# Kernel optimization log

Hardware: AMD Instinct MI355X
Metric: run time of the kernel (lower is better)

## Reference

```python
import jax, jax.numpy as jnp
import numpy as np

# Model dims
B, T, D = 1, 2048, 2048          # batch, seq_len, d_model
HI, DI = 4, 64                   # indexer heads / dim
H, DH = 16, 128                  # attention heads / head dim (H*DH == D)
TOPK = 512                       # sparse top-k tokens per query
NEG = -1e9


def setup_inputs() -> dict:
    key = jax.random.key(0)
    ks = jax.random.split(key, 8)
    s = 0.02  # weight init scale
    return {
        "hidden_states": jax.random.normal(ks[0], (B, T, D), jnp.float32),
        "Wq_idx": jax.random.normal(ks[1], (D, HI * DI), jnp.float32) * s,
        "Wk_idx": jax.random.normal(ks[2], (D, DI), jnp.float32) * s,
        "Ww_idx": jax.random.normal(ks[3], (D, HI), jnp.float32) * s,
        "Wq": jax.random.normal(ks[4], (D, H * DH), jnp.float32) * s,
        "Wk": jax.random.normal(ks[5], (D, H * DH), jnp.float32) * s,
        "Wv": jax.random.normal(ks[6], (D, H * DH), jnp.float32) * s,
        "Wo": jax.random.normal(ks[7], (H * DH, D), jnp.float32) * s,
    }


def reference(hidden_states, Wq_idx, Wk_idx, Ww_idx, Wq, Wk, Wv, Wo):
    x = hidden_states
    # ---- Lightning indexer: I[t,s] = sum_j w[t,j] * relu(q[t,j] . k[s]) ----
    qi = (x @ Wq_idx).reshape(B, T, HI, DI)          # [B,T,HI,DI]
    ki = x @ Wk_idx                                   # [B,S,DI]
    w = x @ Ww_idx                                    # [B,T,HI]
    dots = jnp.einsum('bthd,bsd->bths', qi, ki)       # [B,T,HI,S]
    index_scores = (jax.nn.relu(dots) * w[..., None]).sum(axis=2)  # [B,T,S]

    # ---- Top-k token selection with causal mask ----
    causal = jnp.triu(jnp.ones((T, T), dtype=bool), 1)            # True above diag
    masked_scores = jnp.where(causal[None], NEG, index_scores)
    _, top_idx = jax.lax.top_k(masked_scores, TOPK)               # [B,T,TOPK]
    b_ix = jnp.arange(B)[:, None, None]
    t_ix = jnp.arange(T)[None, :, None]
    top_mask = jnp.zeros((B, T, T), dtype=bool).at[b_ix, t_ix, top_idx].set(True)
    add_mask = jnp.where(top_mask, 0.0, NEG).astype(x.dtype)      # [B,T,S]

    # ---- Dense multi-head attention with additive sparse mask ----
    q = (x @ Wq).reshape(B, T, H, DH)
    k = (x @ Wk).reshape(B, T, H, DH)
    v = (x @ Wv).reshape(B, T, H, DH)
    scores = jnp.einsum('bthd,bshd->bhts', q, k) / np.sqrt(DH).astype(np.float32)
    scores = scores + add_mask[:, None]                            # [B,H,T,S]
    probs = jax.nn.softmax(scores, axis=-1)
    attn = jnp.einsum('bhts,bshd->bthd', probs, v).reshape(B, T, H * DH)
    attn_output = attn @ Wo                                        # [B,T,D]
    return attn_output
```

## Files before the change

kernel.cpp:

```cpp
#include <hip/hip_runtime.h>
#include <cstdint>
#include <cstddef>

#define T_DIM 2048
#define D_DIM 2048
#define HI_N 4
#define DI_N 64
#define H_N 16
#define DH_N 128
#define TOPK_N 512
#define NEG_F (-1e9f)
#define FA_NEG (-1e30f)

typedef __attribute__((ext_vector_type(8))) short short8;
typedef __attribute__((ext_vector_type(4))) float f32x4;
typedef unsigned short ushort_t;

__device__ __forceinline__ unsigned short f2bf(float f) {
  unsigned u = __float_as_uint(f);
  u += 0x7FFFu + ((u >> 16) & 1u);
  return (unsigned short)(u >> 16);
}
__device__ __forceinline__ float bf2f(unsigned short b) {
  return __uint_as_float((unsigned)b << 16);
}

__global__ __launch_bounds__(256) void idx_proj(const float* __restrict__ x,
                                                const float* __restrict__ Wq_idx,
                                                const float* __restrict__ Wk_idx,
                                                const float* __restrict__ Ww_idx,
                                                float* __restrict__ qi,
                                                float* __restrict__ ki,
                                                float* __restrict__ wI) {
  __shared__ float As[2][16][64];
  __shared__ float Bs[2][16][64];
  const int bm = blockIdx.y << 6;
  const int bn_id = blockIdx.x;
  const float* B; float* C; int ldB, cb, ncols;
  if (bn_id < 4)       { B = Wq_idx; C = qi; ldB = 256; cb = bn_id << 6; ncols = 64; }
  else if (bn_id == 4) { B = Wk_idx; C = ki; ldB = 64;  cb = 0;          ncols = 64; }
  else                 { B = Ww_idx; C = wI; ldB = 4;   cb = 0;          ncols = 4;  }
  const int tid = threadIdx.x;
  const int tx = tid & 15, ty = tid >> 4;
  const int am = tid >> 2;
  const int ak = (tid & 3) << 2;
  float acc[4][4] = {};

  float4 a4 = *(const float4*)&x[(size_t)(bm + am) * 2048 + ak];
  float4 b4 = make_float4(0, 0, 0, 0);
  if ((tx << 2) < ncols) b4 = *(const float4*)&B[(size_t)ty * ldB + cb + (tx << 2)];
  As[0][ak + 0][am] = a4.x; As[0][ak + 1][am] = a4.y;
  As[0][ak + 2][am] = a4.z; As[0][ak + 3][am] = a4.w;
  *(float4*)&Bs[0][ty][tx << 2] = b4;

  int p = 0;
  for (int k0 = 0; k0 < 2048; k0 += 16) {
    __syncthreads();
    const bool more = (k0 + 16) < 2048;
    if (more) {
      a4 = *(const float4*)&x[(size_t)(bm + am) * 2048 + k0 + 16 + ak];
      if ((tx << 2) < ncols)
        b4 = *(const float4*)&B[(size_t)(k0 + 16 + ty) * ldB + cb + (tx << 2)];
    }
#pragma unroll
    for (int kk = 0; kk < 16; ++kk) {
      float4 av4 = *(const float4*)&As[p][kk][ty << 2];
      float4 bv4 = *(const float4*)&Bs[p][kk][tx << 2];
      float av[4] = {av4.x, av4.y, av4.z, av4.w};
      float bv[4] = {bv4.x, bv4.y, bv4.z, bv4.w};
#pragma unroll
      for (int i = 0; i < 4; ++i)
#pragma unroll
        for (int j = 0; j < 4; ++j) acc[i][j] += av[i] * bv[j];
    }
    if (more) {
      As[1 - p][ak + 0][am] = a4.x; As[1 - p][ak + 1][am] = a4.y;
      As[1 - p][ak + 2][am] = a4.z; As[1 - p][ak + 3][am] = a4.w;
      *(float4*)&Bs[1 - p][ty][tx << 2] = b4;
    }
    p ^= 1;
  }
#pragma unroll
  for (int i = 0; i < 4; ++i) {
    int m = bm + (ty << 2) + i;
    int n0 = tx << 2;
    if (n0 + 3 < ncols) {
      *(float4*)&C[(size_t)m * ldB + cb + n0] =
          make_float4(acc[i][0], acc[i][1], acc[i][2], acc[i][3]);
    } else {
#pragma unroll
      for (int j = 0; j < 4; ++j)
        if (n0 + j < ncols) C[(size_t)m * ldB + cb + n0 + j] = acc[i][j];
    }
  }
}

__global__ __launch_bounds__(256) void cast_bf16(const float* __restrict__ in,
                                                 ushort_t* __restrict__ out) {
  int i = (blockIdx.x * 256 + threadIdx.x) * 4;
  float4 f = *(const float4*)(in + i);
  ushort4 o;
  o.x = f2bf(f.x); o.y = f2bf(f.y); o.z = f2bf(f.z); o.w = f2bf(f.w);
  *(ushort4*)(out + i) = o;
}

__global__ __launch_bounds__(256) void cast_transpose(const float* __restrict__ in,
                                                      ushort_t* __restrict__ out,
                                                      int R, int C) {
  __shared__ float tile[32][33];
  const int bx = blockIdx.x * 32;
  const int by = blockIdx.y * 32;
  const int tx = threadIdx.x & 31, ty = threadIdx.x >> 5;
#pragma unroll
  for (int i = 0; i < 32; i += 8)
    tile[ty + i][tx] = in[(size_t)(by + ty + i) * C + bx + tx];
  __syncthreads();
#pragma unroll
  for (int i = 0; i < 32; i += 8)
    out[(size_t)(bx + ty + i) * R + by + tx] = f2bf(tile[tx][ty + i]);
}

__global__ __launch_bounds__(256) void transpose_bf(const ushort_t* __restrict__ in,
                                                    ushort_t* __restrict__ out,
                                                    int ldin) {
  __shared__ ushort_t tile[64][68];
  const int bx = blockIdx.x * 64;
  const int by = blockIdx.y * 64;
  const int tid = threadIdx.x;
#pragma unroll
  for (int p = 0; p < 4; ++p) {
    int r = p * 16 + (tid >> 4), c0 = (tid & 15) * 4;
    *(ushort4*)&tile[r][c0] = *(const ushort4*)(in + (size_t)(by + r) * ldin + bx + c0);
  }
  __syncthreads();
#pragma unroll
  for (int p = 0; p < 4; ++p) {
    int r = p * 16 + (tid >> 4), c0 = (tid & 15) * 4;
    ushort4 o;
    o.x = tile[c0 + 0][r]; o.y = tile[c0 + 1][r];
    o.z = tile[c0 + 2][r]; o.w = tile[c0 + 3][r];
    *(ushort4*)(out + (size_t)(bx + r) * T_DIM + by + c0) = o;
  }
}

template <int OUT_BF16>
__global__ __launch_bounds__(256) void gemm_bt(const ushort_t* __restrict__ A,
                                               const ushort_t* __restrict__ Bt,
                                               void* __restrict__ C,
                                               int M, int N, int K) {
  __shared__ __attribute__((aligned(16))) ushort_t As[128 * 64];
  __shared__ __attribute__((aligned(16))) ushort_t Bs[128 * 64];
  const int bm = blockIdx.y << 7;
  const int bn = blockIdx.x << 7;
  const int tid = threadIdx.x;
  const int lane = tid & 63;
  const int wv = tid >> 6;
  const int wm = (wv >> 1) << 6;
  const int wn = (wv & 1) << 6;

  f32x4 acc[4][4] = {};

  const int sr = tid >> 3;
  const int sc = (tid & 7) << 3;
  const ushort_t* ga = A + (size_t)(bm + sr) * K + sc;
  const ushort_t* gb = Bt + (size_t)(bn + sr) * K + sc;
  const size_t rstep = (size_t)32 * K;

  for (int k0 = 0; k0 < K; k0 += 64) {
#pragma unroll
    for (int i = 0; i < 4; ++i) {
      __builtin_amdgcn_global_load_lds(
          (const __attribute__((address_space(1))) unsigned int*)(ga + i * rstep + k0),
          (__attribute__((address_space(3))) unsigned int*)(As + i * 2048 + tid * 8),
          16, 0, 0);
      __builtin_amdgcn_global_load_lds(
          (const __attribute__((address_space(1))) unsigned int*)(gb + i * rstep + k0),
          (__attribute__((address_space(3))) unsigned int*)(Bs + i * 2048 + tid * 8),
          16, 0, 0);
    }
    __syncthreads();
#pragma unroll
    for (int ks = 0; ks < 2; ++ks) {
      short8 af[4], bfr[4];
      const int kk = (ks << 5) + ((lane >> 4) << 3);
#pragma unroll
      for (int i = 0; i < 4; ++i) {
        af[i]  = *(const short8*)(As + (wm + (i << 4) + (lane & 15)) * 64 + kk);
        bfr[i] = *(const short8*)(Bs + (wn + (i << 4) + (lane & 15)) * 64 + kk);
      }
#pragma unroll
      for (int i = 0; i < 4; ++i)
#pragma unroll
        for (int j = 0; j < 4; ++j)
          acc[i][j] = __builtin_amdgcn_mfma_f32_16x16x32_bf16(af[i], bfr[j], acc[i][j], 0, 0, 0);
    }
    __syncthreads();
  }

  const int lrow = (lane >> 4) << 2;
  const int lcol = lane & 15;
#pragma unroll
  for (int i = 0; i < 4; ++i) {
    const int row = bm + wm + (i << 4) + lrow;
#pragma unroll
    for (int j = 0; j < 4; ++j) {
      const int col = bn + wn + (j << 4) + lcol;
#pragma unroll
      for (int r = 0; r < 4; ++r) {
        if (OUT_BF16)
          ((ushort_t*)C)[(size_t)(row + r) * N + col] = f2bf(acc[i][j][r]);
        else
          ((float*)C)[(size_t)(row + r) * N + col] = acc[i][j][r];
      }
    }
  }
}

__global__ __launch_bounds__(256) void idx_scores_rt(const float* __restrict__ qi,
                                                     const float* __restrict__ ki,
                                                     const float* __restrict__ w,
                                                     float* __restrict__ out) {
  const int t0 = blockIdx.y << 6, s0 = blockIdx.x << 6;
  const int tid = threadIdx.x;
  const int tx = tid & 15, ty = tid >> 4;
  if (s0 > t0 + 63) {
    const float4 nf = make_float4(NEG_F, NEG_F, NEG_F, NEG_F);
#pragma unroll
    for (int i = 0; i < 4; ++i) {
      int m = t0 + (ty << 2) + i;
      *(float4*)&out[(size_t)m * T_DIM + s0 + (tx << 2)] = nf;
    }
    return;
  }
  __shared__ float As[16][64];
  __shared__ float Bs[16][64];
  __shared__ float wsh[64][4];
  if (tid < 64) *(float4*)wsh[tid] = *(const float4*)&w[(size_t)(t0 + tid) * 4];
  const int am = tid >> 2;
  const int ak = (tid & 3) << 2;
  float oacc[4][4] = {};
#pragma unroll
  for (int h = 0; h < HI_N; ++h) {
    float dacc[4][4] = {};
    for (int k0 = 0; k0 < DI_N; k0 += 16) {
      float4 qa = *(const float4*)&qi[(size_t)(t0 + am) * 256 + h * DI_N + k0 + ak];
      float4 kb = *(const float4*)&ki[(size_t)(s0 + am) * DI_N + k0 + ak];
      __syncthreads();
      As[ak + 0][am] = qa.x; As[ak + 1][am] = qa.y;
      As[ak + 2][am] = qa.z; As[ak + 3][am] = qa.w;
      Bs[ak + 0][am] = kb.x; Bs[ak + 1][am] = kb.y;
      Bs[ak + 2][am] = kb.z; Bs[ak + 3][am] = kb.w;
      __syncthreads();
#pragma unroll
      for (int kk = 0; kk < 16; ++kk) {
        float4 a4 = *(const float4*)&As[kk][ty << 2];
        float4 b4 = *(const float4*)&Bs[kk][tx << 2];
        float av[4] = {a4.x, a4.y, a4.z, a4.w};
        float bv[4] = {b4.x, b4.y, b4.z, b4.w};
#pragma unroll
        for (int i = 0; i < 4; ++i)
#pragma unroll
          for (int j = 0; j < 4; ++j) dacc[i][j] += av[i] * bv[j];
      }
    }
#pragma unroll
    for (int i = 0; i < 4; ++i) {
      float wh = wsh[(ty << 2) + i][h];
#pragma unroll
      for (int j = 0; j < 4; ++j) oacc[i][j] += fmaxf(dacc[i][j], 0.f) * wh;
    }
  }
#pragma unroll
  for (int i = 0; i < 4; ++i) {
    int m = t0 + (ty << 2) + i;
    int n0 = s0 + (tx << 2);
    float4 r;
    r.x = (n0 + 0 > m) ? NEG_F : oacc[i][0];
    r.y = (n0 + 1 > m) ? NEG_F : oacc[i][1];
    r.z = (n0 + 2 > m) ? NEG_F : oacc[i][2];
    r.w = (n0 + 3 > m) ? NEG_F : oacc[i][3];
    *(float4*)&out[(size_t)m * T_DIM + n0] = r;
  }
}

__global__ __launch_bounds__(256) void select_mask(const float* __restrict__ scores,
                                                   unsigned long long* __restrict__ maskbits) {
  const int t = blockIdx.x, tid = threadIdx.x;
  __shared__ unsigned int hist[256];
  __shared__ unsigned int s_prefix, s_krem;
  __shared__ unsigned char bytes[256];
  unsigned int uv[8];
  const float* row = scores + (size_t)t * T_DIM;
  {
    float4 f0 = *(const float4*)(row + tid * 8);
    float4 f1 = *(const float4*)(row + tid * 8 + 4);
    float fv[8] = {f0.x, f0.y, f0.z, f0.w, f1.x, f1.y, f1.z, f1.w};
#pragma unroll
    for (int j = 0; j < 8; ++j) {
      unsigned u = __float_as_uint(fv[j]);
      uv[j] = (u & 0x80000000u) ? ~u : (u | 0x80000000u);
    }
  }
  if (tid == 0) { s_prefix = 0u; s_krem = TOPK_N; }
  for (int p = 0; p < 4; ++p) {
    const int sh = 24 - 8 * p;
    hist[tid] = 0;
    __syncthreads();
    const unsigned pm = p ? (0xFFFFFFFFu << (32 - 8 * p)) : 0u;
    const unsigned prefix = s_prefix;
#pragma unroll
    for (int j = 0; j < 8; ++j)
      if ((uv[j] & pm) == prefix) atomicAdd(&hist[(uv[j] >> sh) & 255], 1u);
    __syncthreads();
    if (tid == 0) {
      unsigned krem = s_krem, cum = 0;
      int b = 255;
      for (;; --b) { cum += hist[b]; if (cum >= krem) break; }
      s_prefix = prefix | ((unsigned)b << sh);
      s_krem = krem - (cum - hist[b]);
    }
    __syncthreads();
  }
  const unsigned V = s_prefix;
  const int kr = (int)s_krem;
  int eqc = 0;
#pragma unroll
  for (int j = 0; j < 8; ++j) eqc += (uv[j] == V);
  __syncthreads();
  hist[tid] = (unsigned)eqc;
  __syncthreads();
  for (int off = 1; off < 256; off <<= 1) {
    int v = (int)hist[tid];
    if (tid >= off) v += (int)hist[tid - off];
    __syncthreads();
    hist[tid] = (unsigned)v;
    __syncthreads();
  }
  int run = (int)hist[tid] - eqc;
  unsigned char byte = 0;
#pragma unroll
  for (int j = 0; j < 8; ++j) {
    bool eq = (uv[j] == V);
    bool take = (uv[j] > V) || (eq && run < kr);
    run += eq;
    byte |= (unsigned char)(take ? (1u << j) : 0u);
  }
  bytes[tid] = byte;
  __syncthreads();
  if (tid < 32) {
    unsigned long long wqw = 0;
#pragma unroll
    for (int b = 0; b < 8; ++b)
      wqw |= (unsigned long long)bytes[tid * 8 + b] << (8 * b);
    maskbits[(size_t)t * 32 + tid] = wqw;
  }
}

__global__ __launch_bounds__(256, 1) void flash_attn(
    const ushort_t* __restrict__ q, const ushort_t* __restrict__ k,
    const ushort_t* __restrict__ vt, const unsigned long long* __restrict__ maskbits,
    ushort_t* __restrict__ attn, int ldqk) {
  __shared__ __attribute__((aligned(16))) ushort_t Ks[128 * 128];
  __shared__ __attribute__((aligned(16))) ushort_t Vts[128 * 128];
  __shared__ __attribute__((aligned(16))) ushort_t Ps[128 * 136];
  __shared__ float mstate[2][128], lstate[2][128];
  __shared__ float pmax[2][128], psum[2][128];

  const int tt = blockIdx.x;
  const int h  = blockIdx.y;
  const int t0 = tt << 7;
  const int tid = threadIdx.x;
  const int lane = tid & 63;
  const int wv = tid >> 6;
  const int wm = (wv >> 1) << 6;
  const int wn = (wv & 1) << 6;
  const int l15 = lane & 15, l4 = lane >> 4;

  {
    const ushort_t* gq = q + (size_t)(t0 + (tid >> 4)) * ldqk + h * DH_N + (tid & 15) * 8;
#pragma unroll
    for (int p = 0; p < 8; ++p)
      __builtin_amdgcn_global_load_lds(
          (const __attribute__((address_space(1))) unsigned int*)(gq + (size_t)p * 16 * ldqk),
          (__attribute__((address_space(3))) unsigned int*)(Ks + p * 2048 + tid * 8), 16, 0, 0);
  }
  __syncthreads();
  short8 qfrag[4][4];
#pragma unroll
  for (int ks = 0; ks < 4; ++ks)
#pragma unroll
    for (int i = 0; i < 4; ++i)
      qfrag[ks][i] = *(const short8*)(Ks + (wm + i * 16 + l15) * 128 + ks * 32 + l4 * 8);
  if (tid < 128) { mstate[0][tid] = -INFINITY; lstate[0][tid] = 0.f; }

  f32x4 acc[4][4] = {};
  const int nst = (tt < 4) ? 4 : (tt + 1);
  const bool owner = ((wv & 1) == 0) && (l15 == 0);
  const float rsc = 0.08838834764831845f;

  for (int st = 0; st < nst; ++st) {
    const int s0 = st << 7;
    __syncthreads();
    {
      const ushort_t* gk = k + (size_t)(s0 + (tid >> 4)) * ldqk + h * DH_N + (tid & 15) * 8;
      const ushort_t* gv = vt + (size_t)(h * DH_N + (tid >> 4)) * T_DIM + s0 + (tid & 15) * 8;
#pragma unroll
      for (int p = 0; p < 8; ++p) {
        __builtin_amdgcn_global_load_lds(
            (const __attribute__((address_space(1))) unsigned int*)(gk + (size_t)p * 16 * ldqk),
            (__attribute__((address_space(3))) unsigned int*)(Ks + p * 2048 + tid * 8), 16, 0, 0);
        __builtin_amdgcn_global_load_lds(
            (const __attribute__((address_space(1))) unsigned int*)(gv + (size_t)p * 16 * T_DIM),
            (__attribute__((address_space(3))) unsigned int*)(Vts + p * 2048 + tid * 8), 16, 0, 0);
      }
    }
    unsigned long long mw[4][4];
    {
      const int wbase = (s0 >> 6) + (wn >> 6);
#pragma unroll
      for (int i = 0; i < 4; ++i)
#pragma unroll
        for (int r = 0; r < 4; ++r)
          mw[i][r] = maskbits[(size_t)(t0 + wm + i * 16 + l4 * 4 + r) * 32 + wbase];
    }
    __syncthreads();

    f32x4 sacc[4][4] = {};
#pragma unroll
    for (int ks = 0; ks < 4; ++ks) {
      short8 bfr[4];
#pragma unroll
      for (int j = 0; j < 4; ++j)
        bfr[j] = *(const short8*)(Ks + (wn + j * 16 + l15) * 128 + ks * 32 + l4 * 8);
#pragma unroll
      for (int i = 0; i < 4; ++i)
#pragma unroll
        for (int j = 0; j < 4; ++j)
          sacc[i][j] = __builtin_amdgcn_mfma_f32_16x16x32_bf16(qfrag[ks][i], bfr[j], sacc[i][j], 0, 0, 0);
    }
#pragma unroll
    for (int i = 0; i < 4; ++i)
#pragma unroll
      for (int j = 0; j < 4; ++j)
#pragma unroll
        for (int r = 0; r < 4; ++r) {
          bool sel = (mw[i][r] >> (j * 16 + l15)) & 1;
          sacc[i][j][r] = sel ? sacc[i][j][r] * rsc : FA_NEG;
        }
    float pmx[4][4];
#pragma unroll
    for (int i = 0; i < 4; ++i)
#pragma unroll
      for (int r = 0; r < 4; ++r) {
        float m0 = fmaxf(fmaxf(sacc[i][0][r], sacc[i][1][r]), fmaxf(sacc[i][2][r], sacc[i][3][r]));
#pragma unroll
        for (int off = 1; off < 16; off <<= 1) m0 = fmaxf(m0, __shfl_xor(m0, off));
        pmx[i][r] = m0;
      }
    if (l15 == 0)
#pragma unroll
      for (int i = 0; i < 4; ++i)
#pragma unroll
        for (int r = 0; r < 4; ++r)
          pmax[wv & 1][wm + i * 16 + l4 * 4 + r] = pmx[i][r];
    __syncthreads();

    const int rp = st & 1, wp = 1 - rp;
    float nmr[4][4];
#pragma unroll
    for (int i = 0; i < 4; ++i)
#pragma unroll
      for (int r = 0; r < 4; ++r) {
        int rw = wm + i * 16 + l4 * 4 + r;
        nmr[i][r] = fmaxf(mstate[rp][rw], fmaxf(pmax[0][rw], pmax[1][rw]));
      }
    float alpha_c[4];
#pragma unroll
    for (int j = 0; j < 4; ++j) {
      int col = wn + j * 16 + l15;
      float mo = mstate[rp][col];
      float nc = fmaxf(mo, fmaxf(pmax[0][col], pmax[1][col]));
      alpha_c[j] = __expf(mo - nc);
    }
    if (owner)
#pragma unroll
      for (int i = 0; i < 4; ++i)
#pragma unroll
        for (int r = 0; r < 4; ++r)
          mstate[wp][wm + i * 16 + l4 * 4 + r] = nmr[i][r];

    float psr[4][4] = {};
#pragma unroll
    for (int i = 0; i < 4; ++i)
#pragma unroll
      for (int j = 0; j < 4; ++j)
#pragma unroll
        for (int r = 0; r < 4; ++r) {
          float s = sacc[i][j][r];
          float pv = (s <= -1e29f) ? 0.f : __expf(s - nmr[i][r]);
          sacc[i][j][r] = pv;
          psr[i][r] += pv;
        }
#pragma unroll
    for (int i = 0; i < 4; ++i)
#pragma unroll
      for (int j = 0; j < 4; ++j) {
        int col = wn + j * 16 + l15;
#pragma unroll
        for (int r = 0; r < 4; ++r)
          Ps[(wm + i * 16 + l4 * 4 + r) * 136 + col] = f2bf(sacc[i][j][r]);
      }
#pragma unroll
    for (int i = 0; i < 4; ++i)
#pragma unroll
      for (int r = 0; r < 4; ++r) {
        float sv = psr[i][r];
#pragma unroll
        for (int off = 1; off < 16; off <<= 1) sv += __shfl_xor(sv, off);
        psr[i][r] = sv;
      }
    if (l15 == 0)
#pragma unroll
      for (int i = 0; i < 4; ++i)
#pragma unroll
        for (int r = 0; r < 4; ++r)
          psum[wv & 1][wm + i * 16 + l4 * 4 + r] = psr[i][r];
#pragma unroll
    for (int i = 0; i < 4; ++i)
#pragma unroll
      for (int j = 0; j < 4; ++j)
#pragma unroll
        for (int r = 0; r < 4; ++r)
          acc[i][j][r] *= alpha_c[j];
    __syncthreads();

    if (owner)
#pragma unroll
      for (int i = 0; i < 4; ++i)
#pragma unroll
        for (int r = 0; r < 4; ++r) {
          int rw = wm + i * 16 + l4 * 4 + r;
          float al = __expf(mstate[rp][rw] - nmr[i][r]);
          lstate[wp][rw] = al * lstate[rp][rw] + psum[0][rw] + psum[1][rw];
        }
#pragma unroll
    for (int ks = 0; ks < 4; ++ks) {
      short8 af[4], bfr[4];
#pragma unroll
      for (int i = 0; i < 4; ++i)
        af[i] = *(const short8*)(Vts + (wm + i * 16 + l15) * 128 + ks * 32 + l4 * 8);
#pragma unroll
      for (int j = 0; j < 4; ++j)
        bfr[j] = *(const short8*)(Ps + (wn + j * 16 + l15) * 136 + ks * 32 + l4 * 8);
#pragma unroll
      for (int i = 0; i < 4; ++i)
#pragma unroll
        for (int j = 0; j < 4; ++j)
          acc[i][j] = __builtin_amdgcn_mfma_f32_16x16x32_bf16(af[i], bfr[j], acc[i][j], 0, 0, 0);
    }
  }
  __syncthreads();
  const int fp = nst & 1;
  float linv[4];
#pragma unroll
  for (int j = 0; j < 4; ++j) linv[j] = 1.f / lstate[fp][wn + j * 16 + l15];
#pragma unroll
  for (int i = 0; i < 4; ++i)
#pragma unroll
    for (int j = 0; j < 4; ++j) {
      int col = wn + j * 16 + l15;
      int dbase = wm + i * 16 + l4 * 4;
      ushort4 pk;
      pk.x = f2bf(acc[i][j][0] * linv[j]);
      pk.y = f2bf(acc[i][j][1] * linv[j]);
      pk.z = f2bf(acc[i][j][2] * linv[j]);
      pk.w = f2bf(acc[i][j][3] * linv[j]);
      *(ushort4*)(Ps + col * 136 + dbase) = pk;
    }
  __syncthreads();
#pragma unroll
  for (int p = 0; p < 8; ++p) {
    int rw = p * 16 + (tid >> 4);
    int d0 = (tid & 15) * 8;
    *(ulonglong2*)(attn + (size_t)(t0 + rw) * D_DIM + h * DH_N + d0) =
        *(const ulonglong2*)(Ps + rw * 136 + d0);
  }
}

extern "C" void kernel_launch(void* const* d_in, const int* in_sizes, int n_in,
                              void* d_out, int out_size, void* d_ws, size_t ws_size,
                              hipStream_t stream) {
  (void)in_sizes; (void)n_in; (void)out_size; (void)ws_size;
  const float* x      = (const float*)d_in[0];
  const float* Wq_idx = (const float*)d_in[1];
  const float* Wk_idx = (const float*)d_in[2];
  const float* Ww_idx = (const float*)d_in[3];
  const float* Wq     = (const float*)d_in[4];
  const float* Wk     = (const float*)d_in[5];
  const float* Wv     = (const float*)d_in[6];
  const float* Wo     = (const float*)d_in[7];
  float* out = (float*)d_out;

  char* ws = (char*)d_ws;
  const size_t MB = 1ull << 20;
  float*    scores  = (float*)(ws);
  ushort_t* qkv_bf  = (ushort_t*)(ws);
  unsigned long long* maskbits = (unsigned long long*)(ws + 25 * MB + 512 * 1024);
  ushort_t* x_bf    = (ushort_t*)(ws + 26 * MB);
  ushort_t* Wcat_t  = (ushort_t*)(ws + 34 * MB);
  ushort_t* vt_bf   = (ushort_t*)(ws + 34 * MB);
  ushort_t* attn_bf = (ushort_t*)(ws + 42 * MB);
  ushort_t* Wo_t    = (ushort_t*)(ws + 58 * MB);
  float*    qi      = (float*)(ws + 66 * MB);
  float*    ki      = (float*)(ws + 68 * MB);
  float*    wI      = (float*)(ws + 68 * MB + 512 * 1024);

  const dim3 blk(256);
  const dim3 tgrid(D_DIM / 32, D_DIM / 32);

  cast_bf16<<<dim3((D_DIM * T_DIM) / 1024), blk, 0, stream>>>(x, x_bf);
  cast_transpose<<<tgrid, blk, 0, stream>>>(Wq, Wcat_t, D_DIM, D_DIM);
  cast_transpose<<<tgrid, blk, 0, stream>>>(Wk, Wcat_t + (size_t)D_DIM * D_DIM, D_DIM, D_DIM);
  cast_transpose<<<tgrid, blk, 0, stream>>>(Wv, Wcat_t + (size_t)2 * D_DIM * D_DIM, D_DIM, D_DIM);
  cast_transpose<<<tgrid, blk, 0, stream>>>(Wo, Wo_t, D_DIM, D_DIM);

  idx_proj<<<dim3(6, T_DIM / 64), blk, 0, stream>>>(x, Wq_idx, Wk_idx, Ww_idx, qi, ki, wI);
  idx_scores_rt<<<dim3(T_DIM / 64, T_DIM / 64), blk, 0, stream>>>(qi, ki, wI, scores);
  select_mask<<<dim3(T_DIM), blk, 0, stream>>>(scores, maskbits);

  gemm_bt<1><<<dim3(3 * D_DIM / 128, T_DIM / 128), blk, 0, stream>>>(
      x_bf, Wcat_t, qkv_bf, T_DIM, 3 * D_DIM, D_DIM);

  transpose_bf<<<dim3(D_DIM / 64, T_DIM / 64), blk, 0, stream>>>(
      qkv_bf + 2 * D_DIM, vt_bf, 3 * D_DIM);

  flash_attn<<<dim3(T_DIM / 128, H_N), blk, 0, stream>>>(
      qkv_bf, qkv_bf + D_DIM, vt_bf, maskbits, attn_bf, 3 * D_DIM);

  gemm_bt<0><<<dim3(D_DIM / 128, T_DIM / 128), blk, 0, stream>>>(
      attn_bf, Wo_t, out, T_DIM, D_DIM, D_DIM);
}
```

Measured before the change: 599.1 us.

## Reuse K tile for P, XOR-swizzle LDS, and allow two blocks per CU

The flash attention kernel drops its separate P buffer and writes P into the K shared-memory tile once QK^T is done. All tiles use an XOR swizzle on 16-byte chunks instead of padding, to avoid LDS bank conflicts. The PV product is reoriented so rows are queries, making the softmax rescale per row and letting the epilogue write straight to global memory without staging. Launch bounds ask for two blocks per CU, which the smaller LDS footprint allows, at the cost of register pressure and scattered 2-byte global stores.

```diff
diff --git a/kernel.cpp b/kernel.cpp
--- a/kernel.cpp
+++ b/kernel.cpp
@@ -356,13 +356,12 @@
   }
 }
 
-__global__ __launch_bounds__(256, 1) void flash_attn(
+__global__ __launch_bounds__(256, 2) void flash_attn3(
     const ushort_t* __restrict__ q, const ushort_t* __restrict__ k,
     const ushort_t* __restrict__ vt, const unsigned long long* __restrict__ maskbits,
     ushort_t* __restrict__ attn, int ldqk) {
   __shared__ __attribute__((aligned(16))) ushort_t Ks[128 * 128];
   __shared__ __attribute__((aligned(16))) ushort_t Vts[128 * 128];
-  __shared__ __attribute__((aligned(16))) ushort_t Ps[128 * 136];
   __shared__ float mstate[2][128], lstate[2][128];
   __shared__ float pmax[2][128], psum[2][128];
 
@@ -376,8 +375,11 @@
   const int wn = (wv & 1) << 6;
   const int l15 = lane & 15, l4 = lane >> 4;
 
+  const int srow = tid >> 4;
+  const int scol = ((tid & 15) ^ srow) << 3;
+
   {
-    const ushort_t* gq = q + (size_t)(t0 + (tid >> 4)) * ldqk + h * DH_N + (tid & 15) * 8;
+    const ushort_t* gq = q + (size_t)(t0 + srow) * ldqk + h * DH_N + scol;
 #pragma unroll
     for (int p = 0; p < 8; ++p)
       __builtin_amdgcn_global_load_lds(
@@ -390,7 +392,8 @@
   for (int ks = 0; ks < 4; ++ks)
 #pragma unroll
     for (int i = 0; i < 4; ++i)
-      qfrag[ks][i] = *(const short8*)(Ks + (wm + i * 16 + l15) * 128 + ks * 32 + l4 * 8);
+      qfrag[ks][i] = *(const short8*)(Ks + (wm + i * 16 + l15) * 128 +
+                                      (((ks * 4 + l4) ^ l15) << 3));
   if (tid < 128) { mstate[0][tid] = -INFINITY; lstate[0][tid] = 0.f; }
 
   f32x4 acc[4][4] = {};
@@ -402,8 +405,8 @@
     const int s0 = st << 7;
     __syncthreads();
     {
-      const ushort_t* gk = k + (size_t)(s0 + (tid >> 4)) * ldqk + h * DH_N + (tid & 15) * 8;
-      const ushort_t* gv = vt + (size_t)(h * DH_N + (tid >> 4)) * T_DIM + s0 + (tid & 15) * 8;
+      const ushort_t* gk = k + (size_t)(s0 + srow) * ldqk + h * DH_N + scol;
+      const ushort_t* gv = vt + (size_t)(h * DH_N + srow) * T_DIM + s0 + scol;
 #pragma unroll
       for (int p = 0; p < 8; ++p) {
         __builtin_amdgcn_global_load_lds(
@@ -431,7 +434,8 @@
       short8 bfr[4];
 #pragma unroll
       for (int j = 0; j < 4; ++j)
-        bfr[j] = *(const short8*)(Ks + (wn + j * 16 + l15) * 128 + ks * 32 + l4 * 8);
+        bfr[j] = *(const short8*)(Ks + (wn + j * 16 + l15) * 128 +
+                                  (((ks * 4 + l4) ^ l15) << 3));
 #pragma unroll
       for (int i = 0; i < 4; ++i)
 #pragma unroll
@@ -466,22 +470,17 @@
     __syncthreads();
 
     const int rp = st & 1, wp = 1 - rp;
-    float nmr[4][4];
+    float nmr[4][4], alpha_r[4][4];
 #pragma unroll
     for (int i = 0; i < 4; ++i)
 #pragma unroll
       for (int r = 0; r < 4; ++r) {
         int rw = wm + i * 16 + l4 * 4 + r;
-        nmr[i][r] = fmaxf(mstate[rp][rw], fmaxf(pmax[0][rw], pmax[1][rw]));
-      }
-    float alpha_c[4];
-#pragma unroll
-    for (int j = 0; j < 4; ++j) {
-      int col = wn + j * 16 + l15;
-      float mo = mstate[rp][col];
-      float nc = fmaxf(mo, fmaxf(pmax[0][col], pmax[1][col]));
-      alpha_c[j] = __expf(mo - nc);
-    }
+        float mo = mstate[rp][rw];
+        float nm = fmaxf(mo, fmaxf(pmax[0][rw], pmax[1][rw]));
+        nmr[i][r] = nm;
+        alpha_r[i][r] = __expf(mo - nm);
+      }
     if (owner)
 #pragma unroll
       for (int i = 0; i < 4; ++i)
@@ -505,10 +504,13 @@
     for (int i = 0; i < 4; ++i)
 #pragma unroll
       for (int j = 0; j < 4; ++j) {
-        int col = wn + j * 16 + l15;
-#pragma unroll
-        for (int r = 0; r < 4; ++r)
-          Ps[(wm + i * 16 + l4 * 4 + r) * 136 + col] = f2bf(sacc[i][j][r]);
+        const int s = wn + j * 16 + l15;
+        const int sc8 = s >> 3, s7 = s & 7;
+#pragma unroll
+        for (int r = 0; r < 4; ++r) {
+          const int t = wm + i * 16 + l4 * 4 + r;
+          Ks[t * 128 + (((sc8 ^ (t & 15)) << 3) | s7)] = f2bf(sacc[i][j][r]);
+        }
       }
 #pragma unroll
     for (int i = 0; i < 4; ++i)
@@ -531,7 +533,7 @@
       for (int j = 0; j < 4; ++j)
 #pragma unroll
         for (int r = 0; r < 4; ++r)
-          acc[i][j][r] *= alpha_c[j];
+          acc[i][j][r] *= alpha_r[i][r];
     __syncthreads();
 
     if (owner)
@@ -540,18 +542,19 @@
 #pragma unroll
         for (int r = 0; r < 4; ++r) {
           int rw = wm + i * 16 + l4 * 4 + r;
-          float al = __expf(mstate[rp][rw] - nmr[i][r]);
-          lstate[wp][rw] = al * lstate[rp][rw] + psum[0][rw] + psum[1][rw];
+          lstate[wp][rw] = alpha_r[i][r] * lstate[rp][rw] + psum[0][rw] + psum[1][rw];
         }
 #pragma unroll
     for (int ks = 0; ks < 4; ++ks) {
       short8 af[4], bfr[4];
 #pragma unroll
       for (int i = 0; i < 4; ++i)
-        af[i] = *(const short8*)(Vts + (wm + i * 16 + l15) * 128 + ks * 32 + l4 * 8);
+        af[i] = *(const short8*)(Ks + (wm + i * 16 + l15) * 128 +
+                                 (((ks * 4 + l4) ^ l15) << 3));
 #pragma unroll
       for (int j = 0; j < 4; ++j)
-        bfr[j] = *(const short8*)(Ps + (wn + j * 16 + l15) * 136 + ks * 32 + l4 * 8);
+        bfr[j] = *(const short8*)(Vts + (wn + j * 16 + l15) * 128 +
+                                  (((ks * 4 + l4) ^ l15) << 3));
 #pragma unroll
       for (int i = 0; i < 4; ++i)
 #pragma unroll
@@ -561,30 +564,23 @@
   }
   __syncthreads();
   const int fp = nst & 1;
-  float linv[4];
-#pragma unroll
-  for (int j = 0; j < 4; ++j) linv[j] = 1.f / lstate[fp][wn + j * 16 + l15];
+  float linv[4][4];
 #pragma unroll
   for (int i = 0; i < 4; ++i)
 #pragma unroll
+    for (int r = 0; r < 4; ++r)
+      linv[i][r] = 1.f / lstate[fp][wm + i * 16 + l4 * 4 + r];
+#pragma unroll
+  for (int i = 0; i < 4; ++i)
+#pragma unroll
     for (int j = 0; j < 4; ++j) {
-      int col = wn + j * 16 + l15;
-      int dbase = wm + i * 16 + l4 * 4;
-      ushort4 pk;
-      pk.x = f2bf(acc[i][j][0] * linv[j]);
-      pk.y = f2bf(acc[i][j][1] * linv[j]);
-      pk.z = f2bf(acc[i][j][2] * linv[j]);
-      pk.w = f2bf(acc[i][j][3] * linv[j]);
-      *(ushort4*)(Ps + col * 136 + dbase) = pk;
-    }
-  __syncthreads();
-#pragma unroll
-  for (int p = 0; p < 8; ++p) {
-    int rw = p * 16 + (tid >> 4);
-    int d0 = (tid & 15) * 8;
-    *(ulonglong2*)(attn + (size_t)(t0 + rw) * D_DIM + h * DH_N + d0) =
-        *(const ulonglong2*)(Ps + rw * 136 + d0);
-  }
+      const int col = h * DH_N + wn + j * 16 + l15;
+#pragma unroll
+      for (int r = 0; r < 4; ++r) {
+        const int row = t0 + wm + i * 16 + l4 * 4 + r;
+        attn[(size_t)row * D_DIM + col] = f2bf(acc[i][j][r] * linv[i][r]);
+      }
+    }
 }
 
 extern "C" void kernel_launch(void* const* d_in, const int* in_sizes, int n_in,
@@ -634,7 +630,7 @@
   transpose_bf<<<dim3(D_DIM / 64, T_DIM / 64), blk, 0, stream>>>(
       qkv_bf + 2 * D_DIM, vt_bf, 3 * D_DIM);
 
-  flash_attn<<<dim3(T_DIM / 128, H_N), blk, 0, stream>>>(
+  flash_attn3<<<dim3(T_DIM / 128, H_N), blk, 0, stream>>>(
       qkv_bf, qkv_bf + D_DIM, vt_bf, maskbits, attn_bf, 3 * D_DIM);
 
   gemm_bt<0><<<dim3(D_DIM / 128, T_DIM / 128), blk, 0, stream>>>(
```

Result: slower. 840.3 us (+40.3%).
